# Performance work log

Measured on AMD Instinct MI355X. Metric: run time of the kernel, lower is better.

## Reference

```python
import jax, jax.numpy as jnp
import numpy as np

NS = 33  # segments per image: id 0 = background, 1..32 = objects (fixed max-object count)
EPS_GN = 1e-5


def conv2d(x, w, b, pad):
    y = jax.lax.conv_general_dilated(x, w, window_strides=(1, 1),
                                     padding=[(pad, pad), (pad, pad)],
                                     dimension_numbers=('NCHW', 'OIHW', 'NCHW'))
    return y + b[None, :, None, None]


def group_norm(x, gamma, beta, groups):
    B, C, H, W = x.shape
    xg = x.reshape(B, groups, C // groups, H, W)
    mu = xg.mean((2, 3, 4), keepdims=True)
    var = xg.var((2, 3, 4), keepdims=True)
    xn = ((xg - mu) / jnp.sqrt(var + EPS_GN)).reshape(B, C, H, W)
    return xn * gamma[None, :, None, None] + beta[None, :, None, None]


def setup_inputs() -> dict:
    key = jax.random.key(0)
    ks = jax.random.split(key, 10)
    B, Cf, H, W = 4, 512, 128, 128
    std = 0.01
    inp = {
        'x': jax.random.normal(ks[0], (B, Cf, H, W), jnp.float32),
        'masks': jax.random.randint(ks[1], (B, H, W), 0, NS).astype(jnp.int32),
        # coord_conv: Conv2d(2, 64, 1)
        'w_coord': jax.random.normal(ks[2], (64, 2, 1, 1), jnp.float32) * std,
        'b_coord': jnp.zeros((64,), jnp.float32),
        # encoder convs + groupnorms
        'w1': jax.random.normal(ks[3], (256, Cf + 64, 3, 3), jnp.float32) * std,
        'b1': jnp.zeros((256,), jnp.float32),
        'g1': jnp.ones((256,), jnp.float32), 'bt1': jnp.zeros((256,), jnp.float32),
        'w2': jax.random.normal(ks[4], (128, 256, 3, 3), jnp.float32) * std,
        'b2': jnp.zeros((128,), jnp.float32),
        'g2': jnp.ones((128,), jnp.float32), 'bt2': jnp.zeros((128,), jnp.float32),
        'w3': jax.random.normal(ks[5], (64, 128, 3, 3), jnp.float32) * std,
        'b3': jnp.zeros((64,), jnp.float32),
        'g3': jnp.ones((64,), jnp.float32), 'bt3': jnp.zeros((64,), jnp.float32),
        # heads (1x1 convs on pooled [64] vectors == tiny matmuls)
        'w_box': jax.random.normal(ks[6], (7, 64, 1, 1), jnp.float32) * std,
        'b_box': jnp.zeros((7,), jnp.float32),
        'w_conf': jax.random.normal(ks[7], (1, 64, 1, 1), jnp.float32) * std,
        'b_conf': jnp.zeros((1,), jnp.float32),
    }
    return inp


def reference(x, masks, w_coord, b_coord, w1, b1, g1, bt1, w2, b2, g2, bt2,
              w3, b3, g3, bt3, w_box, b_box, w_conf, b_conf):
    B, _, H, W = x.shape
    # coordinate grid: channels are [grid_x, grid_y]
    gy, gx = jnp.meshgrid(jnp.arange(H), jnp.arange(W), indexing='ij')
    grid = jnp.stack([gx, gy], axis=0).astype(x.dtype)            # [2,H,W]
    grid = jnp.broadcast_to(grid[None], (B, 2, H, W))
    grid_feats = jax.nn.relu(conv2d(grid, w_coord, b_coord, 0))   # [B,64,H,W]

    h = jnp.concatenate([x, grid_feats], axis=1)                  # [B,576,H,W]
    h = jax.nn.relu(group_norm(conv2d(h, w1, b1, 1), g1, bt1, 8))
    h = jax.nn.relu(group_norm(conv2d(h, w2, b2, 1), g2, bt2, 4))
    h = jax.nn.relu(group_norm(conv2d(h, w3, b3, 1), g3, bt3, 4))  # [B,64,H,W]

    # per-(image, object-id) masked mean pooling via segment_sum
    C = h.shape[1]
    flat = h.transpose(0, 2, 3, 1).reshape(-1, C)                 # [B*H*W, 64]
    seg = (jnp.arange(B, dtype=jnp.int32)[:, None] * NS
           + masks.reshape(B, -1)).reshape(-1)                    # [B*H*W]
    sums = jax.ops.segment_sum(flat, seg, num_segments=B * NS).reshape(B, NS, C)
    counts = jax.ops.segment_sum(jnp.ones_like(seg, jnp.float32), seg,
                                 num_segments=B * NS).reshape(B, NS, 1)
    # drop background segment 0; safe divide matches the <1e-4 skip (empty slots -> 0 pooled)
    pooled = sums[:, 1:] / jnp.maximum(counts[:, 1:], 1e-4)       # [B,32,64]

    boxes = jnp.einsum('boc,kc->bok', pooled, w_box.reshape(7, C)) + b_box   # [B,32,7]
    scores = jnp.einsum('boc,c->bo', pooled, w_conf.reshape(C)) + b_conf[0]  # [B,32]
    return boxes, scores
```

## Files before the change

kernel.cpp:

```cpp
#include <hip/hip_runtime.h>

typedef unsigned short u16;
typedef unsigned int u32;
typedef __bf16 bf16x8 __attribute__((ext_vector_type(8)));
typedef float f32x4 __attribute__((ext_vector_type(4)));

__device__ __forceinline__ u16 f2bf(float f) {
  u32 u = __float_as_uint(f);
  u += 0x7fffu + ((u >> 16) & 1u);
  return (u16)(u >> 16);
}
__device__ __forceinline__ float bf2f(u16 h) {
  return __uint_as_float(((u32)h) << 16);
}

#define GLD_LDS16(g, l)                                                        \
  __builtin_amdgcn_global_load_lds(                                            \
      (__attribute__((address_space(1))) void*)(g),                            \
      (__attribute__((address_space(3))) void*)(l), 16, 0, 0)

__global__ __launch_bounds__(256) void init_k(float* smallb, u16* in1, u16* in2,
                                              u16* in3) {
  int bid = blockIdx.x;
  if (bid < 35) {
    int i = bid * 256 + threadIdx.x;
    if (i < 8708) smallb[i] = 0.f;
    return;
  }
  u16* buf;
  int C, sub;
  if (bid < 51)      { buf = in1; C = 576; sub = bid - 35; }
  else if (bid < 67) { buf = in2; C = 256; sub = bid - 51; }
  else               { buf = in3; C = 128; sub = bid - 67; }
  int b = sub >> 2, s = sub & 3;
  int npx = (s < 2) ? 130 : 128;
  u32* base = (u32*)(buf + (size_t)b * 130 * 130 * C);
  int C2 = C >> 1;
  int total = npx * C2;
  for (int i = threadIdx.x; i < total; i += 256) {
    int p = i / C2, r = i - p * C2;
    int y, x;
    if (s == 0)      { y = 0;     x = p; }
    else if (s == 1) { y = 129;   x = p; }
    else if (s == 2) { y = p + 1; x = 0; }
    else             { y = p + 1; x = 129; }
    base[(y * 130 + x) * C2 + r] = 0u;
  }
}

__global__ __launch_bounds__(256) void repack_all(const float* __restrict__ w1,
                                                  u16* __restrict__ wp1,
                                                  const float* __restrict__ w2,
                                                  u16* __restrict__ wp2,
                                                  const float* __restrict__ w3,
                                                  u16* __restrict__ wp3) {
  int bid = blockIdx.x;
  const float* src;
  u16* dst;
  int CIN, COUT, total, base;
  if (bid < 5184)      { src = w1; dst = wp1; CIN = 576; COUT = 256; total = 1327104; base = bid; }
  else if (bid < 6336) { src = w2; dst = wp2; CIN = 256; COUT = 128; total = 294912;  base = bid - 5184; }
  else                 { src = w3; dst = wp3; CIN = 128; COUT = 64;  total = 73728;   base = bid - 6336; }
  int idx = base * 256 + threadIdx.x;
  if (idx >= total) return;
  int kc = idx & 31;
  int n = (idx >> 5) % COUT;
  int q = idx / (32 * COUT);
  int dydx = q % 9, cb = q / 9;
  dst[idx] = f2bf(src[((size_t)n * CIN + cb * 32 + kc) * 9 + dydx]);
}

__global__ __launch_bounds__(256) void transpose_x(const float* __restrict__ x,
                                                   const float* __restrict__ wcd,
                                                   const float* __restrict__ bcd,
                                                   u16* __restrict__ in1) {
  const int bid = blockIdx.x;
  const int b = bid >> 8, h = (bid >> 1) & 127, half = bid & 1;
  const int w0 = half * 64;
  const int t = threadIdx.x;
  __shared__ u16 tile[128 * 65];
  __shared__ float swc[128], sbc[64];
  if (t < 128) swc[t] = wcd[t];
  else if (t < 192) sbc[t - 128] = bcd[t - 128];
  const int w = t & 63;
  const int cg = t >> 6;
  const float* xb = x + (((size_t)b * 512) * 128 + h) * 128 + w0 + w;
  u16* ob = in1 + ((size_t)(b * 130 + h + 1) * 130 + (w0 + 1)) * 576;
#pragma unroll 1
  for (int cc = 0; cc < 4; ++cc) {
    const int c0 = cc * 128;
#pragma unroll
    for (int j = 0; j < 32; ++j) {
      int cl = j * 4 + cg;
      tile[cl * 65 + w] = f2bf(xb[(size_t)(c0 + cl) * 16384]);
    }
    __syncthreads();
#pragma unroll
    for (int k = 0; k < 4; ++k) {
      int idx = k * 256 + t;
      int ww = idx >> 4, c8 = (idx & 15) * 8;
      union { uint4 u; u16 s[8]; } o;
#pragma unroll
      for (int i = 0; i < 8; ++i) o.s[i] = tile[(c8 + i) * 65 + ww];
      *(uint4*)(ob + (size_t)ww * 576 + c0 + c8) = o.u;
    }
    __syncthreads();
  }
  const int px = t >> 2, cq = (t & 3) * 16;
  const float fw = (float)(w0 + px), fh = (float)h;
  u16* gp = ob + (size_t)px * 576 + 512 + cq;
#pragma unroll
  for (int j = 0; j < 2; ++j) {
    union { uint4 u; u16 s[8]; } o;
#pragma unroll
    for (int i = 0; i < 8; ++i) {
      int c = cq + j * 8 + i;
      float v = swc[2 * c] * fw + swc[2 * c + 1] * fh + sbc[c];
      o.s[i] = f2bf(fmaxf(v, 0.f));
    }
    *(uint4*)(gp + j * 8) = o.u;
  }
}

template <int CIN, int COUT, int BN>
__global__ __launch_bounds__(256) void conv3x3_k(const u16* __restrict__ in,
                                                 const u16* __restrict__ wp,
                                                 const float* __restrict__ bias,
                                                 u16* __restrict__ out, int Hp,
                                                 int Wp, int py, int px,
                                                 float* __restrict__ stats,
                                                 int gsLog2, int nG) {
  constexpr int CB = CIN / 32;
  constexpr int WN = BN / 2;
  constexpr int NT = WN / 16;
  static_assert(BN == 128 || BN == 64, "");
  __shared__ u16 As[128 * 32];
  __shared__ u16 Bs[BN * 32];
  __shared__ float redS[8], redQ[8];

  const int t = threadIdx.x;
  const int L = gridDim.x;
  const int work = (blockIdx.x & 7) * (L >> 3) + (blockIdx.x >> 3);
  const int xt = work >> 9;
  const int rem = work & 511;
  const int b = rem >> 7, h = rem & 127;
  const int n0 = xt * BN;

  const int lane = t & 63, wv = t >> 6;
  const int wm = wv & 1, wn = wv >> 1;
  const int ln = lane & 15, lq = lane >> 4;

  if (t < 8) { redS[t] = 0.f; redQ[t] = 0.f; }

  f32x4 acc[4][NT];
  const f32x4 zero = {0.f, 0.f, 0.f, 0.f};
#pragma unroll
  for (int i = 0; i < 4; ++i)
#pragma unroll
    for (int j = 0; j < NT; ++j) acc[i][j] = zero;

  const int arow = t >> 2;
  const int csw = (((t & 3) ^ ((t >> 3) & 3))) * 8;
  u16* alds0 = &As[arow * 32 + (t & 3) * 8];
  u16* alds1 = &As[(arow + 64) * 32 + (t & 3) * 8];
  u16* blds0 = &Bs[arow * 32 + (t & 3) * 8];

  const u16* inb = in + (size_t)b * 130 * 130 * CIN;
  const int lsw = (lq ^ ((ln >> 1) & 3)) * 8;

#pragma unroll 1
  for (int cb = 0; cb < CB; ++cb) {
    const int coff = cb * 32 + csw;
#pragma unroll
    for (int dydx = 0; dydx < 9; ++dydx) {
      const int dy = dydx / 3, dx = dydx % 3;
      const u16* rowp = inb + ((h + dy) * 130 + dx) * CIN + coff;
      GLD_LDS16(rowp + arow * CIN, alds0);
      GLD_LDS16(rowp + (arow + 64) * CIN, alds1);
      const u16* wq =
          wp + ((size_t)((cb * 9 + dydx) * COUT) + n0 + arow) * 32 + csw;
      GLD_LDS16(wq, blds0);
      if constexpr (BN == 128)
        GLD_LDS16(wq + 2048, &Bs[2048 + arow * 32 + (t & 3) * 8]);
      __syncthreads();
      bf16x8 fa[4], fb[NT];
#pragma unroll
      for (int i = 0; i < 4; ++i)
        fa[i] = *(const bf16x8*)&As[(wm * 64 + i * 16 + ln) * 32 + lsw];
#pragma unroll
      for (int j = 0; j < NT; ++j)
        fb[j] = *(const bf16x8*)&Bs[(wn * WN + j * 16 + ln) * 32 + lsw];
#pragma unroll
      for (int i = 0; i < 4; ++i)
#pragma unroll
        for (int j = 0; j < NT; ++j)
          acc[i][j] = __builtin_amdgcn_mfma_f32_16x16x32_bf16(fa[i], fb[j],
                                                              acc[i][j], 0, 0, 0);
      __syncthreads();
    }
  }

#pragma unroll
  for (int j = 0; j < NT; ++j) {
    const int n = n0 + wn * WN + j * 16 + ln;
    const float bv = bias[n];
    float sj = 0.f, qj = 0.f;
#pragma unroll
    for (int i = 0; i < 4; ++i) {
#pragma unroll
      for (int r = 0; r < 4; ++r) {
        const int w = wm * 64 + i * 16 + lq * 4 + r;
        u16 st = f2bf(acc[i][j][r] + bv);
        out[((size_t)(b * Hp + h + py) * Wp + (w + px)) * COUT + n] = st;
        float vq = bf2f(st);
        sj += vq;
        qj += vq * vq;
      }
    }
    sj += __shfl_xor(sj, 16, 64);
    sj += __shfl_xor(sj, 32, 64);
    qj += __shfl_xor(qj, 16, 64);
    qj += __shfl_xor(qj, 32, 64);
    if (lq == 0) {
      int gl = (wn * WN + j * 16 + ln) >> gsLog2;
      atomicAdd(&redS[gl], sj);
      atomicAdd(&redQ[gl], qj);
    }
  }
  __syncthreads();
  if (t < (BN >> gsLog2)) {
    int g = (n0 >> gsLog2) + t;
    atomicAdd(&stats[b * nG + g], redS[t]);
    atomicAdd(&stats[4 * nG + b * nG + g], redQ[t]);
  }
}

__global__ __launch_bounds__(256) void gn_norm(u16* __restrict__ buf,
                                               const float* __restrict__ stats,
                                               const float* __restrict__ gamma,
                                               const float* __restrict__ beta,
                                               int C, int gsLog2, int nG,
                                               float invCnt, int Hp, int Wp,
                                               int py, int px) {
  const int t = threadIdx.x;
  const int mt = blockIdx.x;
  const int b = mt >> 7, h = mt & 127;
  __shared__ float la[256], lb[256];
  for (int i = t; i < C; i += 256) {
    int g = i >> gsLog2;
    float mean = stats[b * nG + g] * invCnt;
    float m2 = stats[4 * nG + b * nG + g] * invCnt;
    float rstd = rsqrtf(m2 - mean * mean + 1e-5f);
    float a = gamma[i] * rstd;
    la[i] = a;
    lb[i] = beta[i] - mean * a;
  }
  __syncthreads();
  u16* row = buf + ((size_t)(b * Hp + h + py) * Wp + px) * C;
  const int n8 = 128 * C / 8;
  for (int v = t; v < n8; v += 256) {
    uint4 d = *(uint4*)(row + v * 8);
    int c0 = (v * 8) & (C - 1);
    u16* pp = (u16*)&d;
    union { uint4 u; u16 s[8]; } o;
#pragma unroll
    for (int i = 0; i < 8; ++i) {
      float xx = bf2f(pp[i]);
      float y = la[c0 + i] * xx + lb[c0 + i];
      o.s[i] = f2bf(fmaxf(y, 0.f));
    }
    *(uint4*)(row + v * 8) = o.u;
  }
}

__global__ __launch_bounds__(256) void pool_k(const u16* __restrict__ h3,
                                              const int* __restrict__ masks,
                                              const float* __restrict__ stats,
                                              const float* __restrict__ gamma,
                                              const float* __restrict__ beta,
                                              float* __restrict__ gsum,
                                              float* __restrict__ gcnt) {
  const int t = threadIdx.x;
  const int b = blockIdx.x >> 6, chunk = blockIdx.x & 63;
  __shared__ float ls[33 * 64];
  __shared__ float lc[33];
  for (int i = t; i < 33 * 64; i += 256) ls[i] = 0.f;
  if (t < 33) lc[t] = 0.f;
  const int c = t & 63;
  const int g = c >> 4;
  const float invCnt = 1.f / (16384.f * 16.f);
  float mean = stats[b * 4 + g] * invCnt;
  float m2 = stats[16 + b * 4 + g] * invCnt;
  float rstd = rsqrtf(m2 - mean * mean + 1e-5f);
  const float a = gamma[c] * rstd;
  const float cc = beta[c] - mean * a;
  __syncthreads();
  const int p0 = chunk * 256;
  for (int i = 0; i < 64; ++i) {
    int p = p0 + i * 4 + (t >> 6);
    int id = masks[b * 16384 + p];
    float v = bf2f(h3[((size_t)b * 16384 + p) * 64 + c]);
    v = fmaxf(a * v + cc, 0.f);
    atomicAdd(&ls[id * 64 + c], v);
    if (c == 0) atomicAdd(&lc[id], 1.f);
  }
  __syncthreads();
  for (int i = t; i < 33 * 64; i += 256) atomicAdd(&gsum[b * 2112 + i], ls[i]);
  if (t < 33) atomicAdd(&gcnt[b * 33 + t], lc[t]);
}

__global__ __launch_bounds__(256) void heads_k(const float* __restrict__ gsum,
                                               const float* __restrict__ gcnt,
                                               const float* __restrict__ wbox,
                                               const float* __restrict__ bbox,
                                               const float* __restrict__ wconf,
                                               const float* __restrict__ bconf,
                                               float* __restrict__ out) {
  int idx = blockIdx.x * 256 + threadIdx.x;
  if (idx >= 1024) return;
  if (idx < 896) {
    int b = idx / 224, r = idx % 224;
    int o = r / 7, k = r % 7;
    float inv = 1.f / fmaxf(gcnt[b * 33 + o + 1], 1e-4f);
    const float* ps = gsum + (b * 33 + o + 1) * 64;
    float s = 0.f;
    for (int c = 0; c < 64; ++c) s += ps[c] * wbox[k * 64 + c];
    out[idx] = s * inv + bbox[k];
  } else {
    int i = idx - 896;
    int b = i >> 5, o = i & 31;
    float inv = 1.f / fmaxf(gcnt[b * 33 + o + 1], 1e-4f);
    const float* ps = gsum + (b * 33 + o + 1) * 64;
    float s = 0.f;
    for (int c = 0; c < 64; ++c) s += ps[c] * wconf[c];
    out[896 + i] = s * inv + bconf[0];
  }
}

extern "C" void kernel_launch(void* const* d_in, const int* in_sizes, int n_in,
                              void* d_out, int out_size, void* d_ws,
                              size_t ws_size, hipStream_t stream) {
  (void)in_sizes; (void)n_in; (void)out_size; (void)ws_size;
  const float* x       = (const float*)d_in[0];
  const int*   masks   = (const int*)d_in[1];
  const float* w_coord = (const float*)d_in[2];
  const float* b_coord = (const float*)d_in[3];
  const float* w1  = (const float*)d_in[4];
  const float* b1  = (const float*)d_in[5];
  const float* g1  = (const float*)d_in[6];
  const float* bt1 = (const float*)d_in[7];
  const float* w2  = (const float*)d_in[8];
  const float* b2  = (const float*)d_in[9];
  const float* g2  = (const float*)d_in[10];
  const float* bt2 = (const float*)d_in[11];
  const float* w3  = (const float*)d_in[12];
  const float* b3  = (const float*)d_in[13];
  const float* g3  = (const float*)d_in[14];
  const float* bt3 = (const float*)d_in[15];
  const float* wbox  = (const float*)d_in[16];
  const float* bbox  = (const float*)d_in[17];
  const float* wconf = (const float*)d_in[18];
  const float* bconf = (const float*)d_in[19];
  float* out = (float*)d_out;

  char* ws = (char*)d_ws;
  size_t off = 0;
  auto take = [&](size_t bytes) {
    size_t o = off;
    off += (bytes + 255) & ~(size_t)255;
    return o;
  };
  u16* in1 = (u16*)(ws + take((size_t)4 * 130 * 130 * 576 * 2));
  u16* in2 = (u16*)(ws + take((size_t)4 * 130 * 130 * 256 * 2));
  u16* in3 = (u16*)(ws + take((size_t)4 * 130 * 130 * 128 * 2));
  u16* wp1 = (u16*)(ws + take((size_t)9 * 576 * 256 * 2));
  u16* wp2 = (u16*)(ws + take((size_t)9 * 256 * 128 * 2));
  u16* wp3 = (u16*)(ws + take((size_t)9 * 128 * 64 * 2));
  float* smallb = (float*)(ws + take(8708 * 4));
  u16* h3 = in1;

  float* s1   = smallb;
  float* s2   = smallb + 64;
  float* s3   = smallb + 96;
  float* psum = smallb + 128;
  float* pcnt = smallb + 8576;

  init_k<<<dim3(83), 256, 0, stream>>>(smallb, in1, in2, in3);

  repack_all<<<dim3(6624), 256, 0, stream>>>(w1, wp1, w2, wp2, w3, wp3);

  transpose_x<<<dim3(1024), 256, 0, stream>>>(x, w_coord, b_coord, in1);

  conv3x3_k<576, 256, 128><<<dim3(1024), 256, 0, stream>>>(in1, wp1, b1, in2, 130, 130, 1, 1, s1, 5, 8);
  gn_norm<<<dim3(512), 256, 0, stream>>>(in2, s1, g1, bt1, 256, 5, 8, 1.f / (16384.f * 32.f), 130, 130, 1, 1);

  conv3x3_k<256, 128, 128><<<dim3(512), 256, 0, stream>>>(in2, wp2, b2, in3, 130, 130, 1, 1, s2, 5, 4);
  gn_norm<<<dim3(512), 256, 0, stream>>>(in3, s2, g2, bt2, 128, 5, 4, 1.f / (16384.f * 32.f), 130, 130, 1, 1);

  conv3x3_k<128, 64, 64><<<dim3(512), 256, 0, stream>>>(in3, wp3, b3, h3, 128, 128, 0, 0, s3, 4, 4);

  pool_k<<<dim3(256), 256, 0, stream>>>(h3, masks, s3, g3, bt3, psum, pcnt);
  heads_k<<<dim3(4), 256, 0, stream>>>(psum, pcnt, wbox, bbox, wconf, bconf, out);
}
```

Measured before the change: 637.1 us.

## Stage 3-row input slab in LDS per channel block, read weights directly from global

The conv kernel now loads a 3x130-pixel input slab per 32-channel block into LDS once and reuses it across all nine filter taps, instead of reloading a shifted 128-row tile per tap. This cuts the block barriers from two per tap to two per channel block. Weight fragments are now read straight from global memory (cached) rather than staged through LDS. The risk is global-load latency on the B fragments sitting in the MFMA loop with no prefetch, plus a larger LDS footprint that may lower occupancy.

Measured after the change: 595.9 us. 6.5% less time.

```diff
diff --git a/kernel.cpp b/kernel.cpp
--- a/kernel.cpp
+++ b/kernel.cpp
@@ -127,15 +127,16 @@
                                                  const u16* __restrict__ wp,
                                                  const float* __restrict__ bias,
                                                  u16* __restrict__ out, int Hp,
-                                                 int Wp, int py, int px,
+                                                 int Wp, int opy, int opx,
                                                  float* __restrict__ stats,
                                                  int gsLog2, int nG) {
   constexpr int CB = CIN / 32;
   constexpr int WN = BN / 2;
   constexpr int NT = WN / 16;
+  constexpr int ROWCH = 520;
+  constexpr int NCH = 3 * ROWCH;
   static_assert(BN == 128 || BN == 64, "");
-  __shared__ u16 As[128 * 32];
-  __shared__ u16 Bs[BN * 32];
+  __shared__ u16 As3[3 * 130 * 32];
   __shared__ float redS[8], redQ[8];
 
   const int t = threadIdx.x;
@@ -159,44 +160,45 @@
 #pragma unroll
     for (int j = 0; j < NT; ++j) acc[i][j] = zero;
 
-  const int arow = t >> 2;
-  const int csw = (((t & 3) ^ ((t >> 3) & 3))) * 8;
-  u16* alds0 = &As[arow * 32 + (t & 3) * 8];
-  u16* alds1 = &As[(arow + 64) * 32 + (t & 3) * 8];
-  u16* blds0 = &Bs[arow * 32 + (t & 3) * 8];
-
-  const u16* inb = in + (size_t)b * 130 * 130 * CIN;
-  const int lsw = (lq ^ ((ln >> 1) & 3)) * 8;
+  const u16* inb = in + ((size_t)b * 130 + h) * 130 * CIN;
 
 #pragma unroll 1
   for (int cb = 0; cb < CB; ++cb) {
-    const int coff = cb * 32 + csw;
+    __syncthreads();
+    const u16* slab = inb + cb * 32;
+#pragma unroll
+    for (int it = 0; it < 7; ++it) {
+      int c = it * 256 + t;
+      if (c < NCH) {
+        int r = (c >= 2 * ROWCH) ? 2 : (c >= ROWCH ? 1 : 0);
+        int wch = c - r * ROWCH;
+        int pxi = wch >> 2, q = wch & 3;
+        int qs = q ^ ((pxi >> 1) & 3);
+        GLD_LDS16(slab + (r * 130 + pxi) * CIN + qs * 8, &As3[c * 8]);
+      }
+    }
+    __syncthreads();
+    const u16* wcb =
+        wp + ((size_t)(cb * 9) * COUT + n0 + wn * WN + ln) * 32 + lq * 8;
 #pragma unroll
     for (int dydx = 0; dydx < 9; ++dydx) {
       const int dy = dydx / 3, dx = dydx % 3;
-      const u16* rowp = inb + ((h + dy) * 130 + dx) * CIN + coff;
-      GLD_LDS16(rowp + arow * CIN, alds0);
-      GLD_LDS16(rowp + (arow + 64) * CIN, alds1);
-      const u16* wq =
-          wp + ((size_t)((cb * 9 + dydx) * COUT) + n0 + arow) * 32 + csw;
-      GLD_LDS16(wq, blds0);
-      if constexpr (BN == 128)
-        GLD_LDS16(wq + 2048, &Bs[2048 + arow * 32 + (t & 3) * 8]);
-      __syncthreads();
       bf16x8 fa[4], fb[NT];
 #pragma unroll
-      for (int i = 0; i < 4; ++i)
-        fa[i] = *(const bf16x8*)&As[(wm * 64 + i * 16 + ln) * 32 + lsw];
-#pragma unroll
       for (int j = 0; j < NT; ++j)
-        fb[j] = *(const bf16x8*)&Bs[(wn * WN + j * 16 + ln) * 32 + lsw];
+        fb[j] = *(const bf16x8*)(wcb + (size_t)dydx * COUT * 32 + j * 512);
+#pragma unroll
+      for (int i = 0; i < 4; ++i) {
+        int pxl = dx + wm * 64 + i * 16 + ln;
+        int qs = lq ^ ((pxl >> 1) & 3);
+        fa[i] = *(const bf16x8*)&As3[((dy * 130 + pxl) << 5) + qs * 8];
+      }
 #pragma unroll
       for (int i = 0; i < 4; ++i)
 #pragma unroll
         for (int j = 0; j < NT; ++j)
           acc[i][j] = __builtin_amdgcn_mfma_f32_16x16x32_bf16(fa[i], fb[j],
                                                               acc[i][j], 0, 0, 0);
-      __syncthreads();
     }
   }
 
@@ -211,7 +213,7 @@
       for (int r = 0; r < 4; ++r) {
         const int w = wm * 64 + i * 16 + lq * 4 + r;
         u16 st = f2bf(acc[i][j][r] + bv);
-        out[((size_t)(b * Hp + h + py) * Wp + (w + px)) * COUT + n] = st;
+        out[((size_t)(b * Hp + h + opy) * Wp + (w + opx)) * COUT + n] = st;
         float vq = bf2f(st);
         sj += vq;
         qj += vq * vq;
```
